# Performance work log

Measured on AMD Instinct MI355X. Metric: run time of the kernel, lower is better.

## Reference

```python
import jax, jax.numpy as jnp
import numpy as np

D_MODEL = 1024
N_HEAD = 16
N_BR = 4
DH = D_MODEL // N_HEAD            # 64
H_TOT = N_BR * N_HEAD             # 64
SCALE = float(np.pi / np.sqrt(3.0))
ATTN_SCALE = DH ** -0.5


def _rope(x):
    # x: (B, H, T, Dh). Non-interleaved variant: output is cat of the two rotated halves.
    B, H, T, Dh = x.shape
    inv_freq = 1.0 / (10000.0 ** (jnp.arange(0, Dh, 2, dtype=jnp.float32) / Dh))  # (Dh/2,)
    t = jnp.arange(T, dtype=jnp.float32)
    freqs = t[:, None] * inv_freq[None, :]        # (T, Dh/2)
    cos = jnp.cos(freqs)[None, None]              # (1,1,T,Dh/2)
    sin = jnp.sin(freqs)[None, None]
    x1 = x[..., 0::2]
    x2 = x[..., 1::2]
    return jnp.concatenate([-x2 * sin + x1 * cos, x1 * sin + x2 * cos], axis=-1)


def setup_inputs() -> dict:
    key = jax.random.key(0)
    ks = jax.random.split(key, 8)
    s = 0.02
    B, T = 1, 1024
    return {
        "X": jax.random.normal(ks[0], (B, T, D_MODEL), jnp.float32),
        "Wq": jax.random.normal(ks[1], (D_MODEL, H_TOT * DH), jnp.float32) * s,
        "bq": jnp.zeros((H_TOT * DH,), jnp.float32),
        "Wk": jax.random.normal(ks[2], (D_MODEL, D_MODEL), jnp.float32) * s,
        "bk": jnp.zeros((D_MODEL,), jnp.float32),
        "Wv": jax.random.normal(ks[3], (D_MODEL, H_TOT * DH), jnp.float32) * s,
        "bv": jnp.zeros((H_TOT * DH,), jnp.float32),
        "sink_scalars": jax.random.normal(ks[4], (H_TOT, 1, 1), jnp.float32) * s,
        "v_nulls": jax.random.normal(ks[5], (H_TOT, DH), jnp.float32) * s,
        "Wo": jax.random.normal(ks[6], (D_MODEL, D_MODEL), jnp.float32) * s,
        "bo": jnp.zeros((D_MODEL,), jnp.float32),
    }


def reference(X, Wq, bq, Wk, bk, Wv, bv, sink_scalars, v_nulls, Wo, bo):
    B, T, C = X.shape
    q = (X @ Wq + bq).reshape(B, T, H_TOT, DH).transpose(0, 2, 1, 3)   # (B,H,T,Dh)
    v = (X @ Wv + bv).reshape(B, T, H_TOT, DH).transpose(0, 2, 1, 3)
    k_base = (X @ Wk + bk).reshape(B, T, N_HEAD, DH).transpose(0, 2, 1, 3)  # (B,Nh,T,Dh)
    k = jnp.tile(k_base, (1, N_BR, 1, 1))                               # (B,H,T,Dh)

    q = _rope(q)
    k = _rope(k)

    scores = jnp.einsum('bhtd,bhsd->bhts', q, k) * ATTN_SCALE           # (B,H,T,T)
    key_self = jnp.clip(jnp.sum(k * k, axis=-1), 1e-6, None)            # (B,H,T)
    denom = jnp.sqrt(key_self)[:, :, None, :]                           # (B,H,1,T)
    w = jax.nn.softplus(scores / denom)

    causal = jnp.tril(jnp.ones((T, T), dtype=bool))                     # keep lower triangle
    w = jnp.where(causal[None, None], w, 0.0)
    w = w * jax.nn.sigmoid(SCALE * w)

    sinks = jnp.tanh(sink_scalars).reshape(1, H_TOT, 1, 1) + 1e-6       # (1,H,1,1)
    alpha = 1.0 / (jnp.sum(w, axis=-1, keepdims=True) + sinks + 1e-6)   # (B,H,T,1)
    probs_tokens = w * alpha
    probs_sink = sinks * alpha                                          # (B,H,T,1)

    out_tokens = jnp.einsum('bhts,bhsd->bhtd', probs_tokens, v)
    out_sinks = probs_sink * v_nulls[None, :, None, :]                  # (B,H,T,Dh)
    context = out_tokens + out_sinks                                    # (B,H,T,Dh)

    context = context.reshape(B, N_BR, N_HEAD, T, DH)
    context = context.transpose(0, 1, 3, 2, 4).reshape(B, N_BR, T, C)
    y = context @ Wo + bo                                               # (B,N_BR,T,C)
    return jnp.mean(y, axis=1)


if __name__ == "__main__":
    out = reference(**setup_inputs())
    print(out.shape)
```

## Files before the change

kernel.cpp:

```cpp
#include <hip/hip_runtime.h>
#include <math.h>

#define SILU_SCALE 1.8137993642342178f
#define QKV_N 9216
#define LN2 0.6931471805599453f
#define DNSCALE 0.18033688011112042f

typedef __attribute__((ext_vector_type(8))) short bf16x8;
typedef __attribute__((ext_vector_type(4))) float f32x4;

#if __has_builtin(__builtin_amdgcn_exp2f)
#define EXP2(x) __builtin_amdgcn_exp2f(x)
#else
#define EXP2(x) exp2f(x)
#endif
#if __has_builtin(__builtin_amdgcn_logf)
#define LOG2(x) __builtin_amdgcn_logf(x)
#else
#define LOG2(x) __log2f(x)
#endif

__device__ __forceinline__ unsigned short f2bf(float f){
    union { float f; unsigned int i; } u; u.f = f;
    unsigned int r = u.i + 0x7FFFu + ((u.i >> 16) & 1u);
    return (unsigned short)(r >> 16);
}
__device__ __forceinline__ float bf2f(unsigned short s){
    union { unsigned int i; float f; } u; u.i = ((unsigned int)s) << 16;
    return u.f;
}
__device__ __forceinline__ unsigned int pack_bf2(float lo, float hi){
    unsigned int i0 = __float_as_uint(lo) + 0x8000u;
    unsigned int i1 = __float_as_uint(hi) + 0x8000u;
    return __builtin_amdgcn_perm(i1, i0, 0x07060302u);
}
#if __has_builtin(__builtin_amdgcn_cvt_pk_bf16_f32)
typedef __attribute__((ext_vector_type(2))) __bf16 bfp2;
__device__ __forceinline__ unsigned int pack_bf2f(float lo, float hi){
    bfp2 t = __builtin_amdgcn_cvt_pk_bf16_f32(lo, hi);
    return __builtin_bit_cast(unsigned int, t);
}
#else
__device__ __forceinline__ unsigned int pack_bf2f(float lo, float hi){
    return pack_bf2(lo, hi);
}
#endif

__global__ __launch_bounds__(256) void prep_kernel(
    const float* __restrict__ X,
    const float* __restrict__ Wq, const float* __restrict__ Wk,
    const float* __restrict__ Wv, const float* __restrict__ Wo,
    const float* __restrict__ bq, const float* __restrict__ bk,
    const float* __restrict__ bv,
    unsigned short* __restrict__ Xb, unsigned short* __restrict__ WqkvT,
    unsigned short* __restrict__ WoT, float* __restrict__ qkvb)
{
    __shared__ float t[64][65];
    int b = blockIdx.x;
    const int tid = threadIdx.x;

    if (b >= 2560){
        if (b < 3072){
            int i = ((b - 2560) * 256 + tid) * 8;
            float4 a = *(const float4*)&X[i];
            float4 c = *(const float4*)&X[i + 4];
            union { unsigned short u[8]; uint4 v; } o;
            o.u[0]=f2bf(a.x); o.u[1]=f2bf(a.y); o.u[2]=f2bf(a.z); o.u[3]=f2bf(a.w);
            o.u[4]=f2bf(c.x); o.u[5]=f2bf(c.y); o.u[6]=f2bf(c.z); o.u[7]=f2bf(c.w);
            *(uint4*)&Xb[i] = o.v;
        } else {
            int i = (b - 3072) * 256 + tid;
            float v;
            if (i < 4096) v = bq[i];
            else if (i < 5120) v = bk[i - 4096];
            else v = bv[i - 5120];
            qkvb[i] = v;
        }
        return;
    }

    const float* W; unsigned short* Wt; int N, tiles_x;
    if (b < 1024)      { W = Wq; Wt = WqkvT;                       N = 4096; tiles_x = 64; }
    else if (b < 1280) { b -= 1024; W = Wk; Wt = WqkvT + (size_t)4096*1024; N = 1024; tiles_x = 16; }
    else if (b < 2304) { b -= 1280; W = Wv; Wt = WqkvT + (size_t)5120*1024; N = 4096; tiles_x = 64; }
    else               { b -= 2304; W = Wo; Wt = WoT;              N = 1024; tiles_x = 16; }

    const int k0 = (b / tiles_x) * 64, n0 = (b % tiles_x) * 64;
    const int lr  = tid >> 4;
    const int lc4 = (tid & 15) * 4;
    #pragma unroll
    for (int p = 0; p < 4; p++){
        int r = lr + p * 16;
        float4 v = *(const float4*)&W[(size_t)(k0 + r) * N + n0 + lc4];
        t[lc4+0][r] = v.x; t[lc4+1][r] = v.y;
        t[lc4+2][r] = v.z; t[lc4+3][r] = v.w;
    }
    __syncthreads();
    const int wr  = tid >> 3;
    const int wc8 = (tid & 7) * 8;
    #pragma unroll
    for (int p = 0; p < 2; p++){
        int r = wr + p * 32;
        union { unsigned short u[8]; uint4 v; } o;
        #pragma unroll
        for (int j = 0; j < 8; j++) o.u[j] = f2bf(t[r][wc8 + j]);
        *(uint4*)&Wt[(size_t)(n0 + r) * 1024 + k0 + wc8] = o.v;
    }
}

__global__ __launch_bounds__(256) void gemm_qkv(
    const unsigned short* __restrict__ A,
    const unsigned short* __restrict__ Bt,
    const float* __restrict__ bias,
    unsigned short* __restrict__ C)
{
    constexpr int MT = 4, NT = 3;
    __shared__ unsigned short As[128 * 64];
    __shared__ unsigned short Bs[96 * 64];
    const int tid  = threadIdx.x;
    const int wave = tid >> 6;
    const int lane = tid & 63;
    const int l15  = lane & 15;
    const int quad = lane >> 4;
    const int m0 = blockIdx.y * 128;
    const int n0 = blockIdx.x * 96;
    const int wm = (wave >> 1) * 64;
    const int wn = (wave & 1) * 48;

    const int r0 = tid >> 3;
    const int cc = (tid & 7) ^ (r0 & 7);
    const unsigned short* Ap = A  + (size_t)(m0 + r0) * 1024 + cc * 8;
    const unsigned short* Bp = Bt + (size_t)(n0 + r0) * 1024 + cc * 8;
    constexpr size_t STR = (size_t)32 * 1024;

    f32x4 acc[MT][NT];
    #pragma unroll
    for (int i = 0; i < MT; i++)
        #pragma unroll
        for (int j = 0; j < NT; j++)
            acc[i][j] = (f32x4){0.f, 0.f, 0.f, 0.f};

    uint4 a0 = *(const uint4*)(Ap);
    uint4 a1 = *(const uint4*)(Ap + STR);
    uint4 a2 = *(const uint4*)(Ap + 2 * STR);
    uint4 a3 = *(const uint4*)(Ap + 3 * STR);
    uint4 b0 = *(const uint4*)(Bp);
    uint4 b1 = *(const uint4*)(Bp + STR);
    uint4 b2 = *(const uint4*)(Bp + 2 * STR);

    for (int k0 = 0; k0 < 1024; k0 += 64){
        __syncthreads();
        *(uint4*)&As[(size_t)(0 * 256 + tid) * 8] = a0;
        *(uint4*)&As[(size_t)(1 * 256 + tid) * 8] = a1;
        *(uint4*)&As[(size_t)(2 * 256 + tid) * 8] = a2;
        *(uint4*)&As[(size_t)(3 * 256 + tid) * 8] = a3;
        *(uint4*)&Bs[(size_t)(0 * 256 + tid) * 8] = b0;
        *(uint4*)&Bs[(size_t)(1 * 256 + tid) * 8] = b1;
        *(uint4*)&Bs[(size_t)(2 * 256 + tid) * 8] = b2;

        if (k0 + 64 < 1024){
            const unsigned short* An = Ap + k0 + 64;
            const unsigned short* Bn = Bp + k0 + 64;
            a0 = *(const uint4*)(An);
            a1 = *(const uint4*)(An + STR);
            a2 = *(const uint4*)(An + 2 * STR);
            a3 = *(const uint4*)(An + 3 * STR);
            b0 = *(const uint4*)(Bn);
            b1 = *(const uint4*)(Bn + STR);
            b2 = *(const uint4*)(Bn + 2 * STR);
        }
        __syncthreads();

        #pragma unroll
        for (int ks = 0; ks < 2; ks++){
            bf16x8 af[MT], bfr[NT];
            #pragma unroll
            for (int i = 0; i < MT; i++){
                int row = wm + i * 16 + l15;
                int phys = (ks * 4 + quad) ^ (row & 7);
                af[i] = *(const bf16x8*)&As[row * 64 + phys * 8];
            }
            #pragma unroll
            for (int j = 0; j < NT; j++){
                int row = wn + j * 16 + l15;
                int phys = (ks * 4 + quad) ^ (row & 7);
                bfr[j] = *(const bf16x8*)&Bs[row * 64 + phys * 8];
            }
            #pragma unroll
            for (int i = 0; i < MT; i++)
                #pragma unroll
                for (int j = 0; j < NT; j++)
                    acc[i][j] = __builtin_amdgcn_mfma_f32_16x16x32_bf16(af[i], bfr[j], acc[i][j], 0, 0, 0);
        }
    }
    #pragma unroll
    for (int i = 0; i < MT; i++){
        #pragma unroll
        for (int j = 0; j < NT; j++){
            int col = n0 + wn + j * 16 + l15;
            float bv = bias[col];
            #pragma unroll
            for (int r = 0; r < 4; r++){
                int row = m0 + wm + i * 16 + quad * 4 + r;
                C[(size_t)row * QKV_N + col] = f2bf(acc[i][j][r] + bv);
            }
        }
    }
}

__global__ __launch_bounds__(256) void gemm_wo(
    const unsigned short* __restrict__ A,
    const unsigned short* __restrict__ Bt,
    float* __restrict__ P)
{
    constexpr int MT = 4, NT = 2;
    __shared__ unsigned short As[128 * 64];
    __shared__ unsigned short Bs[64 * 64];
    const int tid  = threadIdx.x;
    const int wave = tid >> 6;
    const int lane = tid & 63;
    const int l15  = lane & 15;
    const int quad = lane >> 4;
    const int m0 = blockIdx.y * 128;
    const int n0 = blockIdx.x * 64;
    const int kz = blockIdx.z;
    const int wm = (wave >> 1) * 64;
    const int wn = (wave & 1) * 32;

    const int r0 = tid >> 3;
    const int cc = (tid & 7) ^ (r0 & 7);
    const int kbeg = kz * 512;
    const unsigned short* Ap = A  + (size_t)(m0 + r0) * 1024 + kbeg + cc * 8;
    const unsigned short* Bp = Bt + (size_t)(n0 + r0) * 1024 + kbeg + cc * 8;
    constexpr size_t STR = (size_t)32 * 1024;

    f32x4 acc[MT][NT];
    #pragma unroll
    for (int i = 0; i < MT; i++)
        #pragma unroll
        for (int j = 0; j < NT; j++)
            acc[i][j] = (f32x4){0.f, 0.f, 0.f, 0.f};

    uint4 a0 = *(const uint4*)(Ap);
    uint4 a1 = *(const uint4*)(Ap + STR);
    uint4 a2 = *(const uint4*)(Ap + 2 * STR);
    uint4 a3 = *(const uint4*)(Ap + 3 * STR);
    uint4 b0 = *(const uint4*)(Bp);
    uint4 b1 = *(const uint4*)(Bp + STR);

    for (int kk = 0; kk < 512; kk += 64){
        __syncthreads();
        *(uint4*)&As[(size_t)(0 * 256 + tid) * 8] = a0;
        *(uint4*)&As[(size_t)(1 * 256 + tid) * 8] = a1;
        *(uint4*)&As[(size_t)(2 * 256 + tid) * 8] = a2;
        *(uint4*)&As[(size_t)(3 * 256 + tid) * 8] = a3;
        *(uint4*)&Bs[(size_t)(0 * 256 + tid) * 8] = b0;
        *(uint4*)&Bs[(size_t)(1 * 256 + tid) * 8] = b1;

        if (kk + 64 < 512){
            const unsigned short* An = Ap + kk + 64;
            const unsigned short* Bn = Bp + kk + 64;
            a0 = *(const uint4*)(An);
            a1 = *(const uint4*)(An + STR);
            a2 = *(const uint4*)(An + 2 * STR);
            a3 = *(const uint4*)(An + 3 * STR);
            b0 = *(const uint4*)(Bn);
            b1 = *(const uint4*)(Bn + STR);
        }
        __syncthreads();

        #pragma unroll
        for (int ks = 0; ks < 2; ks++){
            bf16x8 af[MT], bfr[NT];
            #pragma unroll
            for (int i = 0; i < MT; i++){
                int row = wm + i * 16 + l15;
                int phys = (ks * 4 + quad) ^ (row & 7);
                af[i] = *(const bf16x8*)&As[row * 64 + phys * 8];
            }
            #pragma unroll
            for (int j = 0; j < NT; j++){
                int row = wn + j * 16 + l15;
                int phys = (ks * 4 + quad) ^ (row & 7);
                bfr[j] = *(const bf16x8*)&Bs[row * 64 + phys * 8];
            }
            #pragma unroll
            for (int i = 0; i < MT; i++)
                #pragma unroll
                for (int j = 0; j < NT; j++)
                    acc[i][j] = __builtin_amdgcn_mfma_f32_16x16x32_bf16(af[i], bfr[j], acc[i][j], 0, 0, 0);
        }
    }
    float* Pz = P + (size_t)kz * 1024 * 1024;
    #pragma unroll
    for (int i = 0; i < MT; i++){
        #pragma unroll
        for (int j = 0; j < NT; j++){
            int col = n0 + wn + j * 16 + l15;
            #pragma unroll
            for (int r = 0; r < 4; r++){
                int row = m0 + wm + i * 16 + quad * 4 + r;
                Pz[(size_t)row * 1024 + col] = acc[i][j][r];
            }
        }
    }
}

__global__ void wo_reduce(const float* __restrict__ P, const float* __restrict__ bo,
                          float* __restrict__ out)
{
    int i = (blockIdx.x * 256 + threadIdx.x) * 4;
    float4 a = *(const float4*)&P[i];
    float4 b = *(const float4*)&P[1024 * 1024 + i];
    float4 c = *(const float4*)&bo[i & 1023];
    float4 o;
    o.x = a.x + b.x + c.x; o.y = a.y + b.y + c.y;
    o.z = a.z + b.z + c.z; o.w = a.w + b.w + c.w;
    *(float4*)&out[i] = o;
}

__global__ __launch_bounds__(256) void postproc_kernel(
    unsigned short* __restrict__ qkv, unsigned short* __restrict__ VT)
{
    int b = blockIdx.x;
    const int tid = threadIdx.x;
    if (b < 64){
        int idx = b * 256 + tid;
        int t = idx >> 4, h = idx & 15;
        unsigned short* p = qkv + (size_t)t * QKV_N + 4096 + h * 64;
        uint4 raw[8];
        #pragma unroll
        for (int i = 0; i < 8; i++) raw[i] = *(const uint4*)(p + i * 8);
        const unsigned short* rp = (const unsigned short*)raw;
        float x[64];
        #pragma unroll
        for (int i = 0; i < 64; i++) x[i] = bf2f(rp[i]);
        float ra[32], rb[32];
        float ss = 0.f;
        #pragma unroll
        for (int d = 0; d < 32; d++){
            float inv = EXP2(-(float)d * 0.4152410118609203f);
            float s, c; __sincosf((float)t * inv, &s, &c);
            float x1 = x[2*d], x2 = x[2*d+1];
            float a = x1 * c - x2 * s;
            float bb = x1 * s + x2 * c;
            ss = fmaf(a, a, fmaf(bb, bb, ss));
            ra[d] = a; rb[d] = bb;
        }
        float scale = DNSCALE * rsqrtf(fmaxf(ss, 1e-6f));
        unsigned short o[64];
        #pragma unroll
        for (int d = 0; d < 32; d++){
            o[d]      = f2bf(ra[d] * scale);
            o[d + 32] = f2bf(rb[d] * scale);
        }
        #pragma unroll
        for (int i = 0; i < 8; i++) *(uint4*)(p + i * 8) = ((const uint4*)o)[i];
        return;
    }
    b -= 64;
    const int h = b >> 4, s0 = (b & 15) * 64;
    __shared__ unsigned short tile[64 * 64];
    const unsigned short* V = qkv + 5120;
    const int pr = tid >> 3, cch = tid & 7;
    uint4 g0 = *(const uint4*)&V[(size_t)(s0 + 2 * pr)     * QKV_N + h * 64 + cch * 8];
    uint4 g1 = *(const uint4*)&V[(size_t)(s0 + 2 * pr + 1) * QKV_N + h * 64 + cch * 8];
    const unsigned short* p0 = (const unsigned short*)&g0;
    const unsigned short* p1 = (const unsigned short*)&g1;
    #pragma unroll
    for (int j = 0; j < 8; j++){
        int d = cch * 8 + j;
        int physc = (pr >> 2) ^ ((d ^ (d >> 3)) & 7);
        unsigned int val = (unsigned int)p0[j] | ((unsigned int)p1[j] << 16);
        ((unsigned int*)tile)[d * 32 + physc * 4 + (pr & 3)] = val;
    }
    __syncthreads();
    #pragma unroll
    for (int i = 0; i < 2; i++){
        int slot = tid + i * 256;
        int d = slot >> 3, c = slot & 7;
        int phys = c ^ ((d ^ (d >> 3)) & 7);
        uint4 v = *(const uint4*)&tile[d * 64 + phys * 8];
        *(uint4*)&VT[((size_t)h * 64 + d) * 1024 + s0 + c * 8] = v;
    }
}

__global__ __launch_bounds__(256) void attn_mfma(
    const unsigned short* __restrict__ qkv,
    const unsigned short* __restrict__ VT,
    const float* __restrict__ sinks, const float* __restrict__ vnulls,
    unsigned short* __restrict__ ctx)
{
    __shared__ unsigned short ks[64 * 64];
    __shared__ unsigned short vt[64 * 64];
    __shared__ unsigned short ws[64][72];

    const int tid  = threadIdx.x;
    const int wave = tid >> 6;
    const int lane = tid & 63;
    const int l15  = lane & 15;
    const int quad = lane >> 4;
    const int h  = blockIdx.x;
    const int kh = h & 15;
    const int qt = 15 - blockIdx.y;
    const int t0 = qt << 6;

    const unsigned short* Q  = qkv;
    const unsigned short* Kp = qkv + 4096;
    const unsigned short* Vh = VT + (size_t)h * 64 * 1024;

    const int srow0 = tid >> 3,         sphy0 = tid & 7;
    const int srow1 = (tid + 256) >> 3, sphy1 = tid & 7;
    const int sc0 = sphy0 ^ (srow0 & 7);
    const int sc1 = sphy1 ^ (srow1 & 7);

    bf16x8 qf0, qf1;
    {
        const int t = t0 + wave * 16 + l15;
        const unsigned short* qp = Q + (size_t)t * QKV_N + h * 64 + quad * 16;
        uint4 r0 = *(const uint4*)qp;
        uint4 r1 = *(const uint4*)(qp + 8);
        unsigned short e[16];
        *(uint4*)&e[0] = r0; *(uint4*)&e[8] = r1;
        unsigned short o0[8], o1[8];
        #pragma unroll
        for (int j = 0; j < 8; j++){
            int dp = quad * 8 + j;
            float inv = EXP2(-(float)dp * 0.4152410118609203f);
            float s, c; __sincosf((float)t * inv, &s, &c);
            float x1 = bf2f(e[2*j]), x2 = bf2f(e[2*j+1]);
            o0[j] = f2bf(x1 * c - x2 * s);
            o1[j] = f2bf(x1 * s + x2 * c);
        }
        qf0 = *(const bf16x8*)o0;
        qf1 = *(const bf16x8*)o1;
    }

    bf16x8 ones;
    {
        union { unsigned short u[8]; bf16x8 v; } o;
        #pragma unroll
        for (int j = 0; j < 8; j++) o.u[j] = 0x3F80;
        ones = o.v;
    }

    f32x4 acc_o[4];
    #pragma unroll
    for (int i = 0; i < 4; i++) acc_o[i] = (f32x4){0.f, 0.f, 0.f, 0.f};
    f32x4 acc_den = (f32x4){0.f, 0.f, 0.f, 0.f};
    const int q_glob = t0 + wave * 16 + l15;

    uint4 kr0, kr1, vr0, vr1;
    {
        kr0 = *(const uint4*)&Kp[(size_t)srow0 * QKV_N + kh * 64 + sc0 * 8];
        kr1 = *(const uint4*)&Kp[(size_t)srow1 * QKV_N + kh * 64 + sc1 * 8];
        vr0 = *(const uint4*)&Vh[(size_t)srow0 * 1024 + sc0 * 8];
        vr1 = *(const uint4*)&Vh[(size_t)srow1 * 1024 + sc1 * 8];
    }

    for (int st = 0; st <= qt; st++){
        const int s0 = st << 6;
        __syncthreads();

        *(uint4*)&ks[(size_t)tid * 8]         = kr0;
        *(uint4*)&ks[(size_t)(tid + 256) * 8] = kr1;
        *(uint4*)&vt[(size_t)tid * 8]         = vr0;
        *(uint4*)&vt[(size_t)(tid + 256) * 8] = vr1;

        if (st < qt){
            const int sn = (st + 1) << 6;
            kr0 = *(const uint4*)&Kp[(size_t)(sn + srow0) * QKV_N + kh * 64 + sc0 * 8];
            kr1 = *(const uint4*)&Kp[(size_t)(sn + srow1) * QKV_N + kh * 64 + sc1 * 8];
            vr0 = *(const uint4*)&Vh[(size_t)srow0 * 1024 + sn + sc0 * 8];
            vr1 = *(const uint4*)&Vh[(size_t)srow1 * 1024 + sn + sc1 * 8];
        }
        __syncthreads();

        const bool diag = (st == qt);

        #pragma unroll
        for (int nt = 0; nt < 4; nt++){
            const int sbase = nt * 16 + quad * 4;
            uint2* wp = (uint2*)&ws[wave * 16 + l15][sbase];
            if (diag && nt > wave){ *wp = (uint2){0u, 0u}; continue; }

            f32x4 sc = (f32x4){0.f, 0.f, 0.f, 0.f};
            {
                int srow = nt * 16 + l15;
                int ph0 = quad ^ (srow & 7);
                int ph1 = (4 + quad) ^ (srow & 7);
                bf16x8 kf0 = *(const bf16x8*)&ks[srow * 64 + ph0 * 8];
                bf16x8 kf1 = *(const bf16x8*)&ks[srow * 64 + ph1 * 8];
                sc = __builtin_amdgcn_mfma_f32_16x16x32_bf16(kf0, qf0, sc, 0, 0, 0);
                sc = __builtin_amdgcn_mfma_f32_16x16x32_bf16(kf1, qf1, sc, 0, 0, 0);
            }
            float w4[4];
            if (!diag){
                #pragma unroll
                for (int r = 0; r < 4; r++){
                    float y = sc[r];
                    float p = EXP2(-fabsf(y));
                    float u = fmaxf(y, 0.f) + LOG2(1.f + p);
                    float e3 = EXP2(-SILU_SCALE * u);
                    w4[r] = __fdividef(u, 1.f + e3);
                }
            } else {
                #pragma unroll
                for (int r = 0; r < 4; r++){
                    float y = sc[r];
                    float p = EXP2(-fabsf(y));
                    float u = fmaxf(y, 0.f) + LOG2(1.f + p);
                    float e3 = EXP2(-SILU_SCALE * u);
                    float wv = __fdividef(u, 1.f + e3);
                    w4[r] = (s0 + sbase + r <= q_glob) ? wv : 0.f;
                }
            }
            uint2 pk;
            pk.x = pack_bf2f(w4[0], w4[1]);
            pk.y = pack_bf2f(w4[2], w4[3]);
            *wp = pk;
        }

        {
            const int prow = wave * 16 + l15;
            bf16x8 pf0 = *(const bf16x8*)&ws[prow][quad * 8];
            bf16x8 pf1 = *(const bf16x8*)&ws[prow][32 + quad * 8];
            const bool skip_hi = diag && (wave <= 1);
            #pragma unroll
            for (int dt = 0; dt < 4; dt++){
                int d = dt * 16 + l15;
                int sw = d & 7;
                bf16x8 vf0 = *(const bf16x8*)&vt[d * 64 + (quad ^ sw) * 8];
                acc_o[dt] = __builtin_amdgcn_mfma_f32_16x16x32_bf16(pf0, vf0, acc_o[dt], 0, 0, 0);
                if (!skip_hi){
                    bf16x8 vf1 = *(const bf16x8*)&vt[d * 64 + ((4 + quad) ^ sw) * 8];
                    acc_o[dt] = __builtin_amdgcn_mfma_f32_16x16x32_bf16(pf1, vf1, acc_o[dt], 0, 0, 0);
                }
            }
            acc_den = __builtin_amdgcn_mfma_f32_16x16x32_bf16(pf0, ones, acc_den, 0, 0, 0);
            if (!skip_hi)
                acc_den = __builtin_amdgcn_mfma_f32_16x16x32_bf16(pf1, ones, acc_den, 0, 0, 0);
        }
    }

    float sinkv = tanhf(sinks[h]) + 1e-6f;
    #pragma unroll
    for (int r = 0; r < 4; r++){
        int qg = t0 + wave * 16 + quad * 4 + r;
        float alpha = __fdividef(1.f, LN2 * acc_den[r] + sinkv + 1e-6f);
        #pragma unroll
        for (int dt = 0; dt < 4; dt++){
            int d = dt * 16 + l15;
            float o = (LN2 * acc_o[dt][r] + sinkv * vnulls[h * 64 + d]) * alpha;
            ctx[((size_t)h * 1024 + qg) * 64 + d] = f2bf(o);
        }
    }
}

__global__ void avg_kernel(const unsigned short* __restrict__ ctx, unsigned short* __restrict__ avg)
{
    int i8 = (blockIdx.x * 256 + threadIdx.x) * 8;
    int t = i8 >> 10, c = i8 & 1023;
    int nh = c >> 6, d = c & 63;
    float s[8] = {};
    #pragma unroll
    for (int br = 0; br < 4; br++){
        uint4 v = *(const uint4*)&ctx[((size_t)(br * 16 + nh) * 1024 + t) * 64 + d];
        const unsigned short* p = (const unsigned short*)&v;
        #pragma unroll
        for (int j = 0; j < 8; j++) s[j] += bf2f(p[j]);
    }
    union { unsigned short u[8]; uint4 v; } o;
    #pragma unroll
    for (int j = 0; j < 8; j++) o.u[j] = f2bf(0.25f * s[j]);
    *(uint4*)&avg[i8] = o.v;
}

extern "C" void kernel_launch(void* const* d_in, const int* in_sizes, int n_in,
                              void* d_out, int out_size, void* d_ws, size_t ws_size,
                              hipStream_t stream)
{
    (void)in_sizes; (void)n_in; (void)out_size; (void)ws_size;
    const float* X      = (const float*)d_in[0];
    const float* Wq     = (const float*)d_in[1];
    const float* bq     = (const float*)d_in[2];
    const float* Wk     = (const float*)d_in[3];
    const float* bk     = (const float*)d_in[4];
    const float* Wv     = (const float*)d_in[5];
    const float* bv     = (const float*)d_in[6];
    const float* sinks  = (const float*)d_in[7];
    const float* vnulls = (const float*)d_in[8];
    const float* Wo     = (const float*)d_in[9];
    const float* bo     = (const float*)d_in[10];
    float* out = (float*)d_out;

    unsigned short* w16   = (unsigned short*)d_ws;
    unsigned short* Xb    = w16;
    unsigned short* WqkvT = Xb    + (size_t)1024 * 1024;
    unsigned short* QKVb  = WqkvT + (size_t)QKV_N * 1024;
    unsigned short* WoT   = QKVb  + (size_t)1024 * QKV_N;
    unsigned short* ctxb  = WoT   + (size_t)1024 * 1024;
    unsigned short* avgb  = ctxb  + (size_t)64 * 1024 * 64;
    float* qkvb = (float*)(avgb + (size_t)1024 * 1024);
    unsigned short* VTb = WqkvT;
    float* pWo = (float*)(WqkvT + (size_t)4 * 1024 * 1024);

    dim3 blk(256);
    prep_kernel<<<3108, blk, 0, stream>>>(X, Wq, Wk, Wv, Wo, bq, bk, bv,
                                          Xb, WqkvT, WoT, qkvb);
    gemm_qkv<<<dim3(96, 8), blk, 0, stream>>>(Xb, WqkvT, qkvb, QKVb);
    postproc_kernel<<<1088, blk, 0, stream>>>(QKVb, VTb);
    attn_mfma<<<dim3(64, 16), blk, 0, stream>>>(QKVb, VTb, sinks, vnulls, ctxb);
    avg_kernel<<<512, blk, 0, stream>>>(ctxb, avgb);
    gemm_wo<<<dim3(16, 8, 2), blk, 0, stream>>>(avgb, WoT, pWo);
    wo_reduce<<<1024, blk, 0, stream>>>(pWo, bo, out);
}
```

Measured before the change: 180.9 us.

## Fuse branch averaging and split-K reduction into atomics, drop avg and reduce kernels

The attention kernel now scales its output by 0.25 and atomically accumulates it into an fp32 averaged-context buffer, which replaces the separate bf16 ctx write and the avg kernel. The Wo GEMM reads that fp32 buffer, converts it to bf16 while staging into shared memory, and atomically adds its split-K partials plus half the bias straight into the output, which removes the partial buffer and the reduce kernel. This saves two launches and several intermediate round trips through memory. In exchange it adds two memsets, heavy fp32 atomic traffic with 4-way contention on the context buffer, twice the global read bytes for A in the GEMM, and a summation order that is no longer deterministic.

```diff
diff --git a/kernel.cpp b/kernel.cpp
--- a/kernel.cpp
+++ b/kernel.cpp
@@ -209,9 +209,10 @@
 }
 
 __global__ __launch_bounds__(256) void gemm_wo(
-    const unsigned short* __restrict__ A,
+    const float* __restrict__ Af,
     const unsigned short* __restrict__ Bt,
-    float* __restrict__ P)
+    const float* __restrict__ bo,
+    float* __restrict__ out)
 {
     constexpr int MT = 4, NT = 2;
     __shared__ unsigned short As[128 * 64];
@@ -230,7 +231,7 @@
     const int r0 = tid >> 3;
     const int cc = (tid & 7) ^ (r0 & 7);
     const int kbeg = kz * 512;
-    const unsigned short* Ap = A  + (size_t)(m0 + r0) * 1024 + kbeg + cc * 8;
+    const float* Ap = Af + (size_t)(m0 + r0) * 1024 + kbeg + cc * 8;
     const unsigned short* Bp = Bt + (size_t)(n0 + r0) * 1024 + kbeg + cc * 8;
     constexpr size_t STR = (size_t)32 * 1024;
 
@@ -241,29 +242,40 @@
         for (int j = 0; j < NT; j++)
             acc[i][j] = (f32x4){0.f, 0.f, 0.f, 0.f};
 
-    uint4 a0 = *(const uint4*)(Ap);
-    uint4 a1 = *(const uint4*)(Ap + STR);
-    uint4 a2 = *(const uint4*)(Ap + 2 * STR);
-    uint4 a3 = *(const uint4*)(Ap + 3 * STR);
+    float4 a0l = *(const float4*)(Ap),           a0h = *(const float4*)(Ap + 4);
+    float4 a1l = *(const float4*)(Ap + STR),     a1h = *(const float4*)(Ap + STR + 4);
+    float4 a2l = *(const float4*)(Ap + 2 * STR), a2h = *(const float4*)(Ap + 2 * STR + 4);
+    float4 a3l = *(const float4*)(Ap + 3 * STR), a3h = *(const float4*)(Ap + 3 * STR + 4);
     uint4 b0 = *(const uint4*)(Bp);
     uint4 b1 = *(const uint4*)(Bp + STR);
 
     for (int kk = 0; kk < 512; kk += 64){
         __syncthreads();
-        *(uint4*)&As[(size_t)(0 * 256 + tid) * 8] = a0;
-        *(uint4*)&As[(size_t)(1 * 256 + tid) * 8] = a1;
-        *(uint4*)&As[(size_t)(2 * 256 + tid) * 8] = a2;
-        *(uint4*)&As[(size_t)(3 * 256 + tid) * 8] = a3;
+        {
+            uint4 w;
+            w.x = pack_bf2f(a0l.x, a0l.y); w.y = pack_bf2f(a0l.z, a0l.w);
+            w.z = pack_bf2f(a0h.x, a0h.y); w.w = pack_bf2f(a0h.z, a0h.w);
+            *(uint4*)&As[(size_t)(0 * 256 + tid) * 8] = w;
+            w.x = pack_bf2f(a1l.x, a1l.y); w.y = pack_bf2f(a1l.z, a1l.w);
+            w.z = pack_bf2f(a1h.x, a1h.y); w.w = pack_bf2f(a1h.z, a1h.w);
+            *(uint4*)&As[(size_t)(1 * 256 + tid) * 8] = w;
+            w.x = pack_bf2f(a2l.x, a2l.y); w.y = pack_bf2f(a2l.z, a2l.w);
+            w.z = pack_bf2f(a2h.x, a2h.y); w.w = pack_bf2f(a2h.z, a2h.w);
+            *(uint4*)&As[(size_t)(2 * 256 + tid) * 8] = w;
+            w.x = pack_bf2f(a3l.x, a3l.y); w.y = pack_bf2f(a3l.z, a3l.w);
+            w.z = pack_bf2f(a3h.x, a3h.y); w.w = pack_bf2f(a3h.z, a3h.w);
+            *(uint4*)&As[(size_t)(3 * 256 + tid) * 8] = w;
+        }
         *(uint4*)&Bs[(size_t)(0 * 256 + tid) * 8] = b0;
         *(uint4*)&Bs[(size_t)(1 * 256 + tid) * 8] = b1;
 
         if (kk + 64 < 512){
-            const unsigned short* An = Ap + kk + 64;
+            const float* An = Ap + kk + 64;
             const unsigned short* Bn = Bp + kk + 64;
-            a0 = *(const uint4*)(An);
-            a1 = *(const uint4*)(An + STR);
-            a2 = *(const uint4*)(An + 2 * STR);
-            a3 = *(const uint4*)(An + 3 * STR);
+            a0l = *(const float4*)(An);           a0h = *(const float4*)(An + 4);
+            a1l = *(const float4*)(An + STR);     a1h = *(const float4*)(An + STR + 4);
+            a2l = *(const float4*)(An + 2 * STR); a2h = *(const float4*)(An + 2 * STR + 4);
+            a3l = *(const float4*)(An + 3 * STR); a3h = *(const float4*)(An + 3 * STR + 4);
             b0 = *(const uint4*)(Bn);
             b1 = *(const uint4*)(Bn + STR);
         }
@@ -291,32 +303,19 @@
                     acc[i][j] = __builtin_amdgcn_mfma_f32_16x16x32_bf16(af[i], bfr[j], acc[i][j], 0, 0, 0);
         }
     }
-    float* Pz = P + (size_t)kz * 1024 * 1024;
     #pragma unroll
     for (int i = 0; i < MT; i++){
         #pragma unroll
         for (int j = 0; j < NT; j++){
             int col = n0 + wn + j * 16 + l15;
+            float bv = 0.5f * bo[col];
             #pragma unroll
             for (int r = 0; r < 4; r++){
                 int row = m0 + wm + i * 16 + quad * 4 + r;
-                Pz[(size_t)row * 1024 + col] = acc[i][j][r];
-            }
-        }
-    }
-}
-
-__global__ void wo_reduce(const float* __restrict__ P, const float* __restrict__ bo,
-                          float* __restrict__ out)
-{
-    int i = (blockIdx.x * 256 + threadIdx.x) * 4;
-    float4 a = *(const float4*)&P[i];
-    float4 b = *(const float4*)&P[1024 * 1024 + i];
-    float4 c = *(const float4*)&bo[i & 1023];
-    float4 o;
-    o.x = a.x + b.x + c.x; o.y = a.y + b.y + c.y;
-    o.z = a.z + b.z + c.z; o.w = a.w + b.w + c.w;
-    *(float4*)&out[i] = o;
+                atomicAdd(&out[(size_t)row * 1024 + col], acc[i][j][r] + bv);
+            }
+        }
+    }
 }
 
 __global__ __launch_bounds__(256) void postproc_kernel(
@@ -389,7 +388,7 @@
     const unsigned short* __restrict__ qkv,
     const unsigned short* __restrict__ VT,
     const float* __restrict__ sinks, const float* __restrict__ vnulls,
-    unsigned short* __restrict__ ctx)
+    float* __restrict__ avgf)
 {
     __shared__ unsigned short ks[64 * 64];
     __shared__ unsigned short vt[64 * 64];
@@ -543,37 +542,19 @@
         }
     }
 
+    const int nh = h & 15;
     float sinkv = tanhf(sinks[h]) + 1e-6f;
     #pragma unroll
     for (int r = 0; r < 4; r++){
         int qg = t0 + wave * 16 + quad * 4 + r;
-        float alpha = __fdividef(1.f, LN2 * acc_den[r] + sinkv + 1e-6f);
+        float alpha = __fdividef(0.25f, LN2 * acc_den[r] + sinkv + 1e-6f);
         #pragma unroll
         for (int dt = 0; dt < 4; dt++){
             int d = dt * 16 + l15;
             float o = (LN2 * acc_o[dt][r] + sinkv * vnulls[h * 64 + d]) * alpha;
-            ctx[((size_t)h * 1024 + qg) * 64 + d] = f2bf(o);
-        }
-    }
-}
-
-__global__ void avg_kernel(const unsigned short* __restrict__ ctx, unsigned short* __restrict__ avg)
-{
-    int i8 = (blockIdx.x * 256 + threadIdx.x) * 8;
-    int t = i8 >> 10, c = i8 & 1023;
-    int nh = c >> 6, d = c & 63;
-    float s[8] = {};
-    #pragma unroll
-    for (int br = 0; br < 4; br++){
-        uint4 v = *(const uint4*)&ctx[((size_t)(br * 16 + nh) * 1024 + t) * 64 + d];
-        const unsigned short* p = (const unsigned short*)&v;
-        #pragma unroll
-        for (int j = 0; j < 8; j++) s[j] += bf2f(p[j]);
-    }
-    union { unsigned short u[8]; uint4 v; } o;
-    #pragma unroll
-    for (int j = 0; j < 8; j++) o.u[j] = f2bf(0.25f * s[j]);
-    *(uint4*)&avg[i8] = o.v;
+            atomicAdd(&avgf[(size_t)qg * 1024 + nh * 64 + d], o);
+        }
+    }
 }
 
 extern "C" void kernel_launch(void* const* d_in, const int* in_sizes, int n_in,
@@ -599,19 +580,17 @@
     unsigned short* WqkvT = Xb    + (size_t)1024 * 1024;
     unsigned short* QKVb  = WqkvT + (size_t)QKV_N * 1024;
     unsigned short* WoT   = QKVb  + (size_t)1024 * QKV_N;
-    unsigned short* ctxb  = WoT   + (size_t)1024 * 1024;
-    unsigned short* avgb  = ctxb  + (size_t)64 * 1024 * 64;
-    float* qkvb = (float*)(avgb + (size_t)1024 * 1024);
+    float* avgf = (float*)(WoT + (size_t)1024 * 1024);
+    float* qkvb = (float*)(avgf + (size_t)1024 * 1024);
     unsigned short* VTb = WqkvT;
-    float* pWo = (float*)(WqkvT + (size_t)4 * 1024 * 1024);
 
     dim3 blk(256);
+    hipMemsetAsync(avgf, 0, (size_t)1024 * 1024 * 4, stream);
+    hipMemsetAsync(out,  0, (size_t)1024 * 1024 * 4, stream);
     prep_kernel<<<3108, blk, 0, stream>>>(X, Wq, Wk, Wv, Wo, bq, bk, bv,
                                           Xb, WqkvT, WoT, qkvb);
     gemm_qkv<<<dim3(96, 8), blk, 0, stream>>>(Xb, WqkvT, qkvb, QKVb);
     postproc_kernel<<<1088, blk, 0, stream>>>(QKVb, VTb);
-    attn_mfma<<<dim3(64, 16), blk, 0, stream>>>(QKVb, VTb, sinks, vnulls, ctxb);
-    avg_kernel<<<512, blk, 0, stream>>>(ctxb, avgb);
-    gemm_wo<<<dim3(16, 8, 2), blk, 0, stream>>>(avgb, WoT, pWo);
-    wo_reduce<<<1024, blk, 0, stream>>>(pWo, bo, out);
-}
+    attn_mfma<<<dim3(64, 16), blk, 0, stream>>>(QKVb, VTb, sinks, vnulls, avgf);
+    gemm_wo<<<dim3(16, 8, 2), blk, 0, stream>>>(avgf, WoT, bo, out);
+}
```

New measurement: 191.6 us. 1.06x slower.
